# Kernel optimization log

Hardware: AMD Instinct MI355X
Metric: run time of the kernel (lower is better)

## Reference

```python
import jax, jax.numpy as jnp
import numpy as np

F0_DIM, PH_DIM, MIDI_DIM, DUR_DIM = 64, 128, 64, 64
COND = 256
TOTAL = F0_DIM + PH_DIM + MIDI_DIM + DUR_DIM  # 320
EPS = 1e-5


def setup_inputs() -> dict:
    key = jax.random.key(0)
    ks = jax.random.split(key, 16)
    B, T = 16, 4096
    inp = {
        "f0": jax.random.uniform(ks[0], (B, T), jnp.float32) * 400.0 + 80.0,
        "phone": jax.random.randint(ks[1], (B, T), 0, 100, jnp.int32),
        "duration": jax.random.uniform(ks[2], (B, T), jnp.float32),
        "midi": jax.random.randint(ks[3], (B, T), 0, 128, jnp.int32),
        # f0 encoder: Linear(1,32) -> ReLU -> Linear(32,64)
        "f0_w1": jax.random.normal(ks[4], (1, F0_DIM // 2), jnp.float32) * 0.1,
        "f0_b1": jnp.zeros((F0_DIM // 2,), jnp.float32),
        "f0_w2": jax.random.normal(ks[5], (F0_DIM // 2, F0_DIM), jnp.float32) * 0.1,
        "f0_b2": jnp.zeros((F0_DIM,), jnp.float32),
        # embeddings
        "phone_table": jax.random.normal(ks[6], (100, PH_DIM), jnp.float32),
        "midi_table": jax.random.normal(ks[7], (128, MIDI_DIM), jnp.float32),
        # duration encoder: Linear(1,32) -> ReLU -> Linear(32,64)
        "dur_w1": jax.random.normal(ks[8], (1, DUR_DIM // 2), jnp.float32) * 0.1,
        "dur_b1": jnp.zeros((DUR_DIM // 2,), jnp.float32),
        "dur_w2": jax.random.normal(ks[9], (DUR_DIM // 2, DUR_DIM), jnp.float32) * 0.1,
        "dur_b2": jnp.zeros((DUR_DIM,), jnp.float32),
        # projection: Linear(320,256) -> LayerNorm(256) -> ReLU -> Linear(256,256)
        "proj_w1": jax.random.normal(ks[10], (TOTAL, COND), jnp.float32) * (1.0 / np.sqrt(TOTAL)),
        "proj_b1": jnp.zeros((COND,), jnp.float32),
        "ln_g": jnp.ones((COND,), jnp.float32),
        "ln_b": jnp.zeros((COND,), jnp.float32),
        "proj_w2": jax.random.normal(ks[11], (COND, COND), jnp.float32) * (1.0 / np.sqrt(COND)),
        "proj_b2": jnp.zeros((COND,), jnp.float32),
    }
    return inp


def reference(f0, phone, duration, midi,
              f0_w1, f0_b1, f0_w2, f0_b2,
              phone_table, midi_table,
              dur_w1, dur_b1, dur_w2, dur_b2,
              proj_w1, proj_b1, ln_g, ln_b, proj_w2, proj_b2):
    # f0 / duration MLPs, vectorized over all (batch, time) positions
    f0_h = jax.nn.relu(f0[..., None] * f0_w1[0] + f0_b1)            # [B,T,32]
    f0_emb = f0_h @ f0_w2 + f0_b2                                    # [B,T,64]
    dur_h = jax.nn.relu(duration[..., None] * dur_w1[0] + dur_b1)    # [B,T,32]
    dur_emb = dur_h @ dur_w2 + dur_b2                                # [B,T,64]
    phone_emb = phone_table[phone]                                   # [B,T,128]
    midi_emb = midi_table[midi]                                      # [B,T,64]
    combined = jnp.concatenate([f0_emb, phone_emb, midi_emb, dur_emb], axis=-1)  # [B,T,320]
    h = combined @ proj_w1 + proj_b1                                 # [B,T,256]
    mu = jnp.mean(h, axis=-1, keepdims=True)
    var = jnp.mean((h - mu) ** 2, axis=-1, keepdims=True)
    h = (h - mu) * jax.lax.rsqrt(var + EPS) * ln_g + ln_b
    h = jax.nn.relu(h)
    return h @ proj_w2 + proj_b2                                     # [B,T,256]
```

## Files before the change

### kernel.cpp

```cpp
#include <hip/hip_runtime.h>

typedef _Float16 f16x8 __attribute__((ext_vector_type(8)));
typedef float f32x4 __attribute__((ext_vector_type(4)));
typedef unsigned int u32x2 __attribute__((ext_vector_type(2)));

#define MROWS 65536
#define BM 64
#define NBLK (MROWS / BM)

#define B1F_OFF 0u
#define B2F_OFF 65536u
#define TP_OFF 196608u
#define TM_OFF 299008u
#define BC_OFF 430080u
#define WFD_OFF 431104u


__device__ __forceinline__ unsigned a2off(unsigned X) {
  return (X * 16u) ^ (X & 0x30u);
}

__global__ __launch_bounds__(1024) void prep_tables(
    const float* __restrict__ f0_w2, const float* __restrict__ f0_b2,
    const float* __restrict__ ptab, const float* __restrict__ mtab,
    const float* __restrict__ dur_w2, const float* __restrict__ dur_b2,
    const float* __restrict__ W1, const float* __restrict__ pb1,
    float* __restrict__ wsf) {
  __shared__ float red[4][256];
  const int r = blockIdx.x;
  const int n = threadIdx.x & 255;
  const int ks = threadIdx.x >> 8;
  float s = 0.f;
  if (r < 64) {
    if (r < 32) {
      for (int j = ks * 16; j < ks * 16 + 16; ++j) s = fmaf(f0_w2[r * 64 + j], W1[j * 256 + n], s);
    } else {
      for (int j = ks * 16; j < ks * 16 + 16; ++j)
        s = fmaf(dur_w2[(r - 32) * 64 + j], W1[(256 + j) * 256 + n], s);
    }
  } else if (r < 164) {
    const int p = r - 64;
    for (int j = ks * 32; j < ks * 32 + 32; ++j) s = fmaf(ptab[p * 128 + j], W1[(64 + j) * 256 + n], s);
  } else if (r < 292) {
    const int m = r - 164;
    for (int j = ks * 16; j < ks * 16 + 16; ++j) s = fmaf(mtab[m * 64 + j], W1[(192 + j) * 256 + n], s);
  } else {
    for (int j = ks * 16; j < ks * 16 + 16; ++j) {
      s = fmaf(f0_b2[j], W1[j * 256 + n], s);
      s = fmaf(dur_b2[j], W1[(256 + j) * 256 + n], s);
    }
  }
  red[ks][n] = s;
  __syncthreads();
  if (ks == 0) {
    float t = red[0][n] + red[1][n] + red[2][n] + red[3][n];
    if (r < 64) wsf[WFD_OFF / 4 + r * 256 + n] = t;
    else if (r < 164) wsf[TP_OFF / 4 + (r - 64) * 256 + n] = t;
    else if (r < 292) wsf[TM_OFF / 4 + (r - 164) * 256 + n] = t;
    else wsf[BC_OFF / 4 + n] = t + pb1[n];
  }
}

__global__ __launch_bounds__(64) void prep_frags(const float* __restrict__ W2, char* __restrict__ ws) {
  const float* Wfd = (const float*)(ws + WFD_OFF);
  const int t = blockIdx.x;
  const int l = threadIdx.x;
  const int qq = l >> 4, c = l & 15;
  if (t < 32) {
    const int kt = t >> 4, nt = t & 15;
    const int col = (nt >> 2) * 64 + c * 4 + (nt & 3);
    f16x8 v;
#pragma unroll
    for (int e = 0; e < 8; ++e) {
      const int k = kt * 32 + 4 * qq + (e & 3) + 16 * (e >> 2);
      v[e] = (_Float16)Wfd[k * 256 + col];
    }
    *(f16x8*)(ws + B1F_OFF + (unsigned)((kt * 16 + nt) * 64 + l) * 16u) = v;
  } else {
    const int t2 = t - 32;
    const int kt = t2 >> 4, nt = t2 & 15;
    const int col = (nt >> 2) * 64 + c * 4 + (nt & 3);
    f16x8 v;
#pragma unroll
    for (int e = 0; e < 8; ++e) {
      const int k = kt * 32 + 4 * qq + (e & 3) + 16 * (e >> 2);
      v[e] = (_Float16)W2[k * 256 + col];
    }
    *(f16x8*)(ws + B2F_OFF + (unsigned)((kt * 16 + nt) * 64 + l) * 16u) = v;
  }
}

__global__ __launch_bounds__(256, 3) void cond_enc_main(
    const float* __restrict__ f0g, const int* __restrict__ phone,
    const float* __restrict__ durg, const int* __restrict__ midi,
    const float* __restrict__ f0_w1, const float* __restrict__ f0_b1,
    const float* __restrict__ dur_w1, const float* __restrict__ dur_b1,
    const float* __restrict__ ln_g, const float* __restrict__ ln_b,
    const float* __restrict__ pb2, const char* __restrict__ ws,
    float* __restrict__ out) {
  __shared__ __align__(16) unsigned char smem[32768 + 1024];
  unsigned char* Pbuf = smem;
  float* partials = (float*)(smem + 32768);

  const int tid = threadIdx.x;
  const int l = tid & 63;
  const int w = tid >> 6;
  const int wi = w & 1;
  const int wh = w >> 1;
  const int q = l >> 4;
  const int c = l & 15;
  const int rowbase = blockIdx.x * BM;

  const float* Tp = (const float*)(ws + TP_OFF);
  const float* Tm = (const float*)(ws + TM_OFF);

  const float xf_all = f0g[rowbase + l];
  const float xd_all = durg[rowbase + l];
  const int ph_all = phone[rowbase + l];
  const int md_all = midi[rowbase + l];

  f16x8 a1[2][2];
#pragma unroll
  for (int i = 0; i < 2; ++i) {
    const float xf = __shfl(xf_all, wi * 32 + i * 16 + c);
    const float xd = __shfl(xd_all, wi * 32 + i * 16 + c);
#pragma unroll
    for (int kh = 0; kh < 2; ++kh) {
      f16x8 v;
#pragma unroll
      for (int e = 0; e < 8; ++e) {
        const int ki = 4 * q + (e & 3) + 16 * (e >> 2);
        const float wv = kh ? dur_w1[ki] : f0_w1[ki];
        const float bv = kh ? dur_b1[ki] : f0_b1[ki];
        const float x = kh ? xd : xf;
        v[e] = (_Float16)fmaxf(fmaf(x, wv, bv), 0.f);
      }
      a1[i][kh] = v;
    }
  }

  const f32x4 zero4 = {0.f, 0.f, 0.f, 0.f};
  f32x4 acc1[2][8];
#pragma unroll
  for (int i = 0; i < 2; ++i)
#pragma unroll
    for (int j = 0; j < 8; ++j) acc1[i][j] = zero4;
  {
    const f16x8* B1p = (const f16x8*)(ws + B1F_OFF);
#pragma unroll
    for (int kt = 0; kt < 2; ++kt) {
#pragma unroll
      for (int jc = 0; jc < 2; ++jc) {
        f16x8 bfr[4];
#pragma unroll
        for (int j = 0; j < 4; ++j) bfr[j] = B1p[(kt * 16 + wh * 8 + jc * 4 + j) * 64 + l];
#pragma unroll
        for (int i = 0; i < 2; ++i)
#pragma unroll
          for (int j = 0; j < 4; ++j)
            acc1[i][jc * 4 + j] =
                __builtin_amdgcn_mfma_f32_16x16x32_f16(a1[i][kt], bfr[j], acc1[i][jc * 4 + j], 0, 0, 0);
      }
    }
  }

  const float* bcp = (const float*)(ws + BC_OFF);
#pragma unroll
  for (int i = 0; i < 2; ++i) {
#pragma unroll
    for (int r = 0; r < 4; ++r) {
      const int rrel = wi * 32 + i * 16 + q * 4 + r;
      const int ph = __shfl(ph_all, rrel);
      const int md = __shfl(md_all, rrel);
      float s = 0.f, ss = 0.f;
#pragma unroll
      for (int gl = 0; gl < 2; ++gl) {
        const int g = wh * 2 + gl;
        const f32x4 tp4 = *(const f32x4*)(Tp + ph * 256 + g * 64 + c * 4);
        const f32x4 tm4 = *(const f32x4*)(Tm + md * 256 + g * 64 + c * 4);
        const f32x4 bc4 = *(const f32x4*)(bcp + g * 64 + c * 4);
#pragma unroll
        for (int bq = 0; bq < 4; ++bq) {
          float v = acc1[i][4 * gl + bq][r] + bc4[bq] + tp4[bq] + tm4[bq];
          acc1[i][4 * gl + bq][r] = v;
          s += v;
          ss = fmaf(v, v, ss);
        }
      }
#pragma unroll
      for (int m = 1; m < 16; m <<= 1) {
        s += __shfl_xor(s, m, 64);
        ss += __shfl_xor(ss, m, 64);
      }
      if (c == 0) {
        partials[rrel * 4 + wh * 2 + 0] = s;
        partials[rrel * 4 + wh * 2 + 1] = ss;
      }
    }
  }
  __syncthreads();

  const int lp_base = 16 * (c & 3);
  const unsigned hoff = (unsigned)((c >> 2) & 1) * 8u;
#pragma unroll
  for (int i = 0; i < 2; ++i) {
#pragma unroll
    for (int r = 0; r < 4; ++r) {
      const int rrel = wi * 32 + i * 16 + q * 4 + r;
      const int it = wi * 2 + i;
      const f32x4 pr = *(const f32x4*)(partials + rrel * 4);
      const float s = pr[0] + pr[2];
      const float ss = pr[1] + pr[3];
      const float mu = s * (1.f / 256.f);
      const float var = fmaxf(ss * (1.f / 256.f) - mu * mu, 0.f);
      const float rstd = rsqrtf(var + 1e-5f);
#pragma unroll
      for (int gl = 0; gl < 2; ++gl) {
        const int g = wh * 2 + gl;
        const f32x4 g4 = *(const f32x4*)(ln_g + g * 64 + c * 4);
        const f32x4 lb4 = *(const f32x4*)(ln_b + g * 64 + c * 4);
        unsigned short hw[4];
#pragma unroll
        for (int bq = 0; bq < 4; ++bq) {
          float v = fmaf((acc1[i][4 * gl + bq][r] - mu) * rstd, g4[bq], lb4[bq]);
          v = fmaxf(v, 0.f);
          hw[bq] = __builtin_bit_cast(unsigned short, (_Float16)v);
        }
        u32x2 pkt;
        pkt[0] = (unsigned)hw[0] | ((unsigned)hw[1] << 16);
        pkt[1] = (unsigned)hw[2] | ((unsigned)hw[3] << 16);
        const int kt = 2 * g + (c >> 3);
        const unsigned X = (unsigned)((kt * 4 + it) * 64 + (q * 4 + r + lp_base));
        *(u32x2*)(Pbuf + a2off(X) + hoff) = pkt;
      }
    }
  }
  __syncthreads();

  f32x4 acc2[4][4];
#pragma unroll
  for (int it = 0; it < 4; ++it)
#pragma unroll
    for (int j = 0; j < 4; ++j) acc2[it][j] = zero4;
  {
    const f16x8* B2p = (const f16x8*)(ws + B2F_OFF);
#pragma unroll
    for (int kt = 0; kt < 8; ++kt) {
      f16x8 av[4], bfr[4];
#pragma unroll
      for (int it = 0; it < 4; ++it)
        av[it] = *(const f16x8*)(Pbuf + a2off((unsigned)((kt * 4 + it) * 64 + l)));
#pragma unroll
      for (int j = 0; j < 4; ++j) bfr[j] = B2p[(kt * 16 + w * 4 + j) * 64 + l];
#pragma unroll
      for (int it = 0; it < 4; ++it)
#pragma unroll
        for (int j = 0; j < 4; ++j)
          acc2[it][j] = __builtin_amdgcn_mfma_f32_16x16x32_f16(av[it], bfr[j], acc2[it][j], 0, 0, 0);
    }
  }

  const f32x4 b24 = *(const f32x4*)(pb2 + w * 64 + c * 4);
#pragma unroll
  for (int it = 0; it < 4; ++it)
#pragma unroll
    for (int r = 0; r < 4; ++r) {
      const int grow = rowbase + it * 16 + q * 4 + r;
      f32x4 st;
#pragma unroll
      for (int j = 0; j < 4; ++j) st[j] = acc2[it][j][r] + b24[j];
      __builtin_nontemporal_store(st, (f32x4*)(out + grow * 256 + w * 64 + c * 4));
    }
}

extern "C" void kernel_launch(void* const* d_in, const int* in_sizes, int n_in,
                              void* d_out, int out_size, void* d_ws, size_t ws_size,
                              hipStream_t stream) {
  (void)in_sizes; (void)n_in; (void)out_size; (void)ws_size;
  const float* f0 = (const float*)d_in[0];
  const int* phone = (const int*)d_in[1];
  const float* dur = (const float*)d_in[2];
  const int* midi = (const int*)d_in[3];
  const float* f0_w1 = (const float*)d_in[4];
  const float* f0_b1 = (const float*)d_in[5];
  const float* f0_w2 = (const float*)d_in[6];
  const float* f0_b2 = (const float*)d_in[7];
  const float* ptab = (const float*)d_in[8];
  const float* mtab = (const float*)d_in[9];
  const float* dur_w1 = (const float*)d_in[10];
  const float* dur_b1 = (const float*)d_in[11];
  const float* dur_w2 = (const float*)d_in[12];
  const float* dur_b2 = (const float*)d_in[13];
  const float* W1 = (const float*)d_in[14];
  const float* pb1 = (const float*)d_in[15];
  const float* ln_g = (const float*)d_in[16];
  const float* ln_b = (const float*)d_in[17];
  const float* W2 = (const float*)d_in[18];
  const float* pb2 = (const float*)d_in[19];
  char* ws = (char*)d_ws;
  float* out = (float*)d_out;

  prep_tables<<<293, 1024, 0, stream>>>(f0_w2, f0_b2, ptab, mtab, dur_w2, dur_b2, W1, pb1, (float*)ws);
  prep_frags<<<160, 64, 0, stream>>>(W2, ws);
  cond_enc_main<<<NBLK, 256, 0, stream>>>(f0, phone, dur, midi, f0_w1, f0_b1, dur_w1, dur_b1,
                                          ln_g, ln_b, pb2, ws, out);
}
```

Before: 37.87 us.

## Store phone/midi projected tables in fp16 and split second GEMM into halves

The precomputed phone and midi projection tables are now stored as fp16 instead of fp32, which halves the bytes gathered per row in the main kernel; they are converted back to fp32 on load. The second GEMM is split into two halves of 32 rows each, with the stores issued after each half, so fewer accumulator registers are live and stores can overlap the remaining MFMA work. The cost is a small loss of precision in the table values and the B2 fragments being loaded twice.

```diff
diff --git a/kernel.cpp b/kernel.cpp
--- a/kernel.cpp
+++ b/kernel.cpp
@@ -1,6 +1,7 @@
 #include <hip/hip_runtime.h>
 
 typedef _Float16 f16x8 __attribute__((ext_vector_type(8)));
+typedef _Float16 f16x4 __attribute__((ext_vector_type(4)));
 typedef float f32x4 __attribute__((ext_vector_type(4)));
 typedef unsigned int u32x2 __attribute__((ext_vector_type(2)));
 
@@ -10,8 +11,8 @@
 
 #define B1F_OFF 0u
 #define B2F_OFF 65536u
-#define TP_OFF 196608u
-#define TM_OFF 299008u
+#define TP16_OFF 196608u
+#define TM16_OFF 247808u
 #define BC_OFF 430080u
 #define WFD_OFF 431104u
 
@@ -54,9 +55,10 @@
   __syncthreads();
   if (ks == 0) {
     float t = red[0][n] + red[1][n] + red[2][n] + red[3][n];
+    char* wsb = (char*)wsf;
     if (r < 64) wsf[WFD_OFF / 4 + r * 256 + n] = t;
-    else if (r < 164) wsf[TP_OFF / 4 + (r - 64) * 256 + n] = t;
-    else if (r < 292) wsf[TM_OFF / 4 + (r - 164) * 256 + n] = t;
+    else if (r < 164) ((_Float16*)(wsb + TP16_OFF))[(r - 64) * 256 + n] = (_Float16)t;
+    else if (r < 292) ((_Float16*)(wsb + TM16_OFF))[(r - 164) * 256 + n] = (_Float16)t;
     else wsf[BC_OFF / 4 + n] = t + pb1[n];
   }
 }
@@ -111,8 +113,8 @@
   const int c = l & 15;
   const int rowbase = blockIdx.x * BM;
 
-  const float* Tp = (const float*)(ws + TP_OFF);
-  const float* Tm = (const float*)(ws + TM_OFF);
+  const _Float16* Tp = (const _Float16*)(ws + TP16_OFF);
+  const _Float16* Tm = (const _Float16*)(ws + TM16_OFF);
 
   const float xf_all = f0g[rowbase + l];
   const float xd_all = durg[rowbase + l];
@@ -176,8 +178,10 @@
 #pragma unroll
       for (int gl = 0; gl < 2; ++gl) {
         const int g = wh * 2 + gl;
-        const f32x4 tp4 = *(const f32x4*)(Tp + ph * 256 + g * 64 + c * 4);
-        const f32x4 tm4 = *(const f32x4*)(Tm + md * 256 + g * 64 + c * 4);
+        const f32x4 tp4 =
+            __builtin_convertvector(*(const f16x4*)(Tp + ph * 256 + g * 64 + c * 4), f32x4);
+        const f32x4 tm4 =
+            __builtin_convertvector(*(const f16x4*)(Tm + md * 256 + g * 64 + c * 4), f32x4);
         const f32x4 bc4 = *(const f32x4*)(bcp + g * 64 + c * 4);
 #pragma unroll
         for (int bq = 0; bq < 4; ++bq) {
@@ -237,40 +241,40 @@
   }
   __syncthreads();
 
-  f32x4 acc2[4][4];
-#pragma unroll
-  for (int it = 0; it < 4; ++it)
-#pragma unroll
-    for (int j = 0; j < 4; ++j) acc2[it][j] = zero4;
-  {
-    const f16x8* B2p = (const f16x8*)(ws + B2F_OFF);
+  const f32x4 b24 = *(const f32x4*)(pb2 + w * 64 + c * 4);
+  const f16x8* B2p = (const f16x8*)(ws + B2F_OFF);
+#pragma unroll
+  for (int half = 0; half < 2; ++half) {
+    f32x4 acc2[2][4];
+#pragma unroll
+    for (int i = 0; i < 2; ++i)
+#pragma unroll
+      for (int j = 0; j < 4; ++j) acc2[i][j] = zero4;
 #pragma unroll
     for (int kt = 0; kt < 8; ++kt) {
-      f16x8 av[4], bfr[4];
-#pragma unroll
-      for (int it = 0; it < 4; ++it)
-        av[it] = *(const f16x8*)(Pbuf + a2off((unsigned)((kt * 4 + it) * 64 + l)));
+      f16x8 av[2], bfr[4];
+#pragma unroll
+      for (int i = 0; i < 2; ++i)
+        av[i] = *(const f16x8*)(Pbuf + a2off((unsigned)((kt * 4 + half * 2 + i) * 64 + l)));
 #pragma unroll
       for (int j = 0; j < 4; ++j) bfr[j] = B2p[(kt * 16 + w * 4 + j) * 64 + l];
 #pragma unroll
-      for (int it = 0; it < 4; ++it)
+      for (int i = 0; i < 2; ++i)
 #pragma unroll
         for (int j = 0; j < 4; ++j)
-          acc2[it][j] = __builtin_amdgcn_mfma_f32_16x16x32_f16(av[it], bfr[j], acc2[it][j], 0, 0, 0);
-    }
-  }
-
-  const f32x4 b24 = *(const f32x4*)(pb2 + w * 64 + c * 4);
-#pragma unroll
-  for (int it = 0; it < 4; ++it)
-#pragma unroll
-    for (int r = 0; r < 4; ++r) {
-      const int grow = rowbase + it * 16 + q * 4 + r;
-      f32x4 st;
-#pragma unroll
-      for (int j = 0; j < 4; ++j) st[j] = acc2[it][j][r] + b24[j];
-      __builtin_nontemporal_store(st, (f32x4*)(out + grow * 256 + w * 64 + c * 4));
-    }
+          acc2[i][j] = __builtin_amdgcn_mfma_f32_16x16x32_f16(av[i], bfr[j], acc2[i][j], 0, 0, 0);
+    }
+#pragma unroll
+    for (int i = 0; i < 2; ++i)
+#pragma unroll
+      for (int r = 0; r < 4; ++r) {
+        const int grow = rowbase + (half * 2 + i) * 16 + q * 4 + r;
+        f32x4 st;
+#pragma unroll
+        for (int j = 0; j < 4; ++j) st[j] = acc2[i][j][r] + b24[j];
+        __builtin_nontemporal_store(st, (f32x4*)(out + grow * 256 + w * 64 + c * 4));
+      }
+  }
 }
 
 extern "C" void kernel_launch(void* const* d_in, const int* in_sizes, int n_in,
```

New measurement: 41.12 us. 8.6% more time.
